# Kernel optimization log

Hardware: AMD Instinct MI355X
Metric: run time of the kernel (lower is better)

## Reference

```python
import jax, jax.numpy as jnp
import numpy as np

N_NODES = 50000
N_EDGES = 800000
K_HOPS = 3


def _gcn_norm(edge_index, num_nodes):
    # PyG gcn_norm with add_self_loops=False: sym normalization by target-degree
    row, col = edge_index[0], edge_index[1]  # source j -> target i
    ones = jnp.ones((edge_index.shape[1],), dtype=jnp.float32)
    deg = jax.ops.segment_sum(ones, col, num_segments=num_nodes)
    dinv = jnp.where(deg > 0, 1.0 / jnp.sqrt(deg), 0.0)
    return dinv[row] * dinv[col]  # [E]


def _propagate(h, row, col, norm, num_nodes):
    # out_i = sum_{j->i} norm_e * h_j   (scatter-add over edges)
    msg = h[row] * norm[:, None]  # [E, d]
    return jax.ops.segment_sum(msg, col, num_segments=num_nodes)


def _tag_conv(x, W, b, row, col, norm, num_nodes):
    # out = sum_{k=0..K} (A_norm^k x) @ W[k] + b
    out = x @ W[0]
    h = x
    for k in range(1, K_HOPS + 1):
        h = _propagate(h, row, col, norm, num_nodes)
        out = out + h @ W[k]
    return out + b


def setup_inputs() -> dict:
    key = jax.random.key(0)
    ks = jax.random.split(key, 12)
    x = jax.random.normal(ks[0], (N_NODES, 16), dtype=jnp.float32)
    edge_index = jax.random.randint(ks[1], (2, N_EDGES), 0, N_NODES, dtype=jnp.int64)
    dims = [(16, 64), (64, 64), (64, 64), (64, 64), (64, 4)]
    inp = {"x": x, "edge_index": edge_index}
    for i, (din, dout) in enumerate(dims):
        scale = 1.0 / np.sqrt(din)
        inp[f"W{i}"] = jax.random.normal(ks[2 + 2 * i], (K_HOPS + 1, din, dout), dtype=jnp.float32) * scale
        inp[f"b{i}"] = jnp.zeros((dout,), dtype=jnp.float32)
    return inp


def reference(x, edge_index, W0, b0, W1, b1, W2, b2, W3, b3, W4, b4):
    num_nodes = x.shape[0]
    row, col = edge_index[0], edge_index[1]
    norm = _gcn_norm(edge_index, num_nodes)
    Ws = [W0, W1, W2, W3, W4]
    bs = [b0, b1, b2, b3, b4]
    h = x
    for i in range(4):  # first len(convs)-1 layers: conv -> dropout(identity, eval) -> relu
        h = _tag_conv(h, Ws[i], bs[i], row, col, norm, num_nodes)
        h = jax.nn.relu(h)
    return _tag_conv(h, Ws[4], bs[4], row, col, norm, num_nodes)
```

## Files before the change

kernel.cpp:

```cpp
#include <hip/hip_runtime.h>
#include <hip/hip_fp16.h>

typedef _Float16 f16x8 __attribute__((ext_vector_type(8)));
typedef float f32x4 __attribute__((ext_vector_type(4)));

union H2I { int i; __half2 h; };
static __device__ inline float2 i2f2(int v) {
    H2I u; u.i = v; return __half22float2(u.h);
}
static __device__ inline int f2i2(float a, float b) {
    H2I u; u.h = __floats2half2_rn(a, b); return u.i;
}

struct F8 { float2 a, b, c, d; };
static __device__ inline void fma8(F8& s, int4 g, float w) {
    float2 t;
    t = i2f2(g.x); s.a.x += w * t.x; s.a.y += w * t.y;
    t = i2f2(g.y); s.b.x += w * t.x; s.b.y += w * t.y;
    t = i2f2(g.z); s.c.x += w * t.x; s.c.y += w * t.y;
    t = i2f2(g.w); s.d.x += w * t.x; s.d.y += w * t.y;
}


__global__ __launch_bounds__(256) void count_rank_kernel(const int* __restrict__ col,
                                                         int* __restrict__ cnt,
                                                         unsigned short* __restrict__ rank,
                                                         int E) {
    int e = blockIdx.x * 256 + threadIdx.x;
    if (e < E) rank[e] = (unsigned short)atomicAdd(&cnt[col[e]], 1);
}

__global__ __launch_bounds__(256) void scan_block_kernel(const int* __restrict__ cnt,
                                                         int* __restrict__ off,
                                                         int* __restrict__ bsum, int n) {
    const int gid = blockIdx.x * 256 + threadIdx.x;
    const int v = (gid < n) ? cnt[gid] : 0;
    const int lane = threadIdx.x & 63, w = threadIdx.x >> 6;
    int x = v;
#pragma unroll
    for (int d = 1; d < 64; d <<= 1) {
        int t = __shfl_up(x, d);
        if (lane >= d) x += t;
    }
    __shared__ int wt[4];
    if (lane == 63) wt[w] = x;
    __syncthreads();
    int base = 0;
#pragma unroll
    for (int i = 0; i < 3; ++i)
        if (i < w) base += wt[i];
    const int incl = base + x;
    if (gid < n) off[gid] = incl - v;
    if (threadIdx.x == 255) bsum[blockIdx.x] = incl;
}

__global__ __launch_bounds__(256) void scan_bsum_kernel(const int* __restrict__ bsum,
                                                        int* __restrict__ bbase, int nb) {
    const int tid = threadIdx.x;
    const int v = (tid < nb) ? bsum[tid] : 0;
    const int lane = tid & 63, w = tid >> 6;
    int x = v;
#pragma unroll
    for (int d = 1; d < 64; d <<= 1) {
        int t = __shfl_up(x, d);
        if (lane >= d) x += t;
    }
    __shared__ int wt[4];
    if (lane == 63) wt[w] = x;
    __syncthreads();
    int base = 0;
#pragma unroll
    for (int i = 0; i < 3; ++i)
        if (i < w) base += wt[i];
    if (tid < nb) bbase[tid] = base + x - v;
}

__global__ __launch_bounds__(256) void scan_apply_kernel(int* __restrict__ off,
                                                         const int* __restrict__ bbase,
                                                         int n, int E) {
    const int gid = blockIdx.x * 256 + threadIdx.x;
    if (gid < n) off[gid] += bbase[blockIdx.x];
    if (gid == n) off[n] = E;
}

__global__ __launch_bounds__(256) void prep_kernel(const int* __restrict__ cnt,
                                                   float* __restrict__ dinv,
                                                   const float* __restrict__ x,
                                                   __half* __restrict__ xcat,
                                                   const float* __restrict__ W0,
                                                   const float* __restrict__ W1,
                                                   const float* __restrict__ W2,
                                                   const float* __restrict__ W3,
                                                   __half* __restrict__ Bp0,
                                                   __half* __restrict__ Bp1,
                                                   __half* __restrict__ Bp2,
                                                   __half* __restrict__ Bp3, int N) {
    int t = blockIdx.x * 256 + threadIdx.x;
    if (t < N) {
        const int c = cnt[t];
        dinv[t] = (c > 0) ? 1.0f / sqrtf((float)c) : 0.0f;
        return;
    }
    t -= N;
    if (t < 2 * N) {
        const int n = t >> 1, q = t & 1;
        const float4 v0 = ((const float4*)x)[n * 4 + q * 2 + 0];
        const float4 v1 = ((const float4*)x)[n * 4 + q * 2 + 1];
        int4 o;
        o.x = f2i2(v0.x, v0.y);
        o.y = f2i2(v0.z, v0.w);
        o.z = f2i2(v1.x, v1.y);
        o.w = f2i2(v1.z, v1.w);
        ((int4*)xcat)[n * 8 + q] = o;
        return;
    }
    t -= 2 * N;
    const float* W;
    __half* Bp;
    if (t < 512) {
        W = W0; Bp = Bp0;
    } else if (t < 512 + 2048) {
        W = W1; Bp = Bp1; t -= 512;
    } else if (t < 512 + 2 * 2048) {
        W = W2; Bp = Bp2; t -= 512 + 2048;
    } else if (t < 512 + 3 * 2048) {
        W = W3; Bp = Bp3; t -= 512 + 2 * 2048;
    } else {
        return;
    }
    const int kk = t >> 8;
    const int nt = (t >> 6) & 3;
    const int l = t & 63;
    const int m = l & 15, kg = l >> 4;
    const int col = nt * 16 + m;
    __half tmp[8];
#pragma unroll
    for (int j = 0; j < 8; ++j) {
        const int k = kk * 32 + kg * 8 + j;
        tmp[j] = __float2half(W[k * 64 + col]);
    }
    ((int4*)Bp)[t] = *(int4*)tmp;
}

__global__ __launch_bounds__(256) void scatter_kernel(const int* __restrict__ row,
                                                      const int* __restrict__ col,
                                                      const int* __restrict__ off,
                                                      const unsigned short* __restrict__ rank,
                                                      const float* __restrict__ dinv,
                                                      int2* __restrict__ recs, int E) {
    int e = blockIdx.x * 256 + threadIdx.x;
    if (e >= E) return;
    const int r = row[e], c = col[e];
    const int pos = off[c] + (int)rank[e];
    recs[pos] = make_int2(r, __float_as_int(dinv[r] * dinv[c]));
}


template <int DQ, int S4>
__global__ __launch_bounds__(256) void gatherh_kernel(const int* __restrict__ off,
                                                      const int2* __restrict__ recs,
                                                      const __half* __restrict__ hin,
                                                      __half* __restrict__ hout, int nNodes) {
    const int t = blockIdx.x * 256 + threadIdx.x;
    const int n = t / DQ;
    const int q = t & (DQ - 1);
    if (n >= nNodes) return;
    const int4* __restrict__ h4 = (const int4*)hin;
    F8 s = {};
    int e = off[n];
    const int e1 = off[n + 1];
    for (; e + 8 <= e1; e += 8) {
        const int2 r0 = recs[e + 0];
        const int2 r1 = recs[e + 1];
        const int2 r2 = recs[e + 2];
        const int2 r3 = recs[e + 3];
        const int2 r4 = recs[e + 4];
        const int2 r5 = recs[e + 5];
        const int2 r6 = recs[e + 6];
        const int2 r7 = recs[e + 7];
        const int4 g0 = h4[r0.x * S4 + q];
        const int4 g1 = h4[r1.x * S4 + q];
        const int4 g2 = h4[r2.x * S4 + q];
        const int4 g3 = h4[r3.x * S4 + q];
        const int4 g4 = h4[r4.x * S4 + q];
        const int4 g5 = h4[r5.x * S4 + q];
        const int4 g6 = h4[r6.x * S4 + q];
        const int4 g7 = h4[r7.x * S4 + q];
        fma8(s, g0, __int_as_float(r0.y));
        fma8(s, g1, __int_as_float(r1.y));
        fma8(s, g2, __int_as_float(r2.y));
        fma8(s, g3, __int_as_float(r3.y));
        fma8(s, g4, __int_as_float(r4.y));
        fma8(s, g5, __int_as_float(r5.y));
        fma8(s, g6, __int_as_float(r6.y));
        fma8(s, g7, __int_as_float(r7.y));
    }
    for (; e + 4 <= e1; e += 4) {
        const int2 r0 = recs[e + 0];
        const int2 r1 = recs[e + 1];
        const int2 r2 = recs[e + 2];
        const int2 r3 = recs[e + 3];
        const int4 g0 = h4[r0.x * S4 + q];
        const int4 g1 = h4[r1.x * S4 + q];
        const int4 g2 = h4[r2.x * S4 + q];
        const int4 g3 = h4[r3.x * S4 + q];
        fma8(s, g0, __int_as_float(r0.y));
        fma8(s, g1, __int_as_float(r1.y));
        fma8(s, g2, __int_as_float(r2.y));
        fma8(s, g3, __int_as_float(r3.y));
    }
    for (; e < e1; ++e) {
        const int2 r = recs[e];
        fma8(s, h4[r.x * S4 + q], __int_as_float(r.y));
    }
    int4 o;
    o.x = f2i2(s.a.x, s.a.y);
    o.y = f2i2(s.b.x, s.b.y);
    o.z = f2i2(s.c.x, s.c.y);
    o.w = f2i2(s.d.x, s.d.y);
    ((int4*)hout)[n * S4 + q] = o;
}


template <int K>
__global__ __launch_bounds__(256) void gemmcat_mfma(const __half* __restrict__ A,
                                                    const __half* __restrict__ Bp,
                                                    const float* __restrict__ bias,
                                                    __half* __restrict__ out, int N) {
    __shared__ __half hs[128][72];
    const int wave = threadIdx.x >> 6;
    const int lane = threadIdx.x & 63;
    const int nb = blockIdx.x * 128 + wave * 32;
    const int m = lane & 15;
    const int kg = lane >> 4;

    const int row0 = min(nb + m, N - 1);
    const int row1 = min(nb + 16 + m, N - 1);
    const f16x8* a0p = (const f16x8*)(A + (size_t)row0 * K + kg * 8);
    const f16x8* a1p = (const f16x8*)(A + (size_t)row1 * K + kg * 8);
    const f16x8* bp = (const f16x8*)Bp + lane;

    f32x4 acc[2][4];
#pragma unroll
    for (int nt = 0; nt < 4; ++nt) {
        const float bv = bias[nt * 16 + m];
        acc[0][nt] = (f32x4){bv, bv, bv, bv};
        acc[1][nt] = (f32x4){bv, bv, bv, bv};
    }

#pragma unroll
    for (int kk = 0; kk < K / 32; ++kk) {
        const f16x8 a0 = a0p[kk * 4];
        const f16x8 a1 = a1p[kk * 4];
#pragma unroll
        for (int nt = 0; nt < 4; ++nt) {
            const f16x8 b = bp[(kk * 4 + nt) * 64];
            acc[0][nt] = __builtin_amdgcn_mfma_f32_16x16x32_f16(a0, b, acc[0][nt], 0, 0, 0);
            acc[1][nt] = __builtin_amdgcn_mfma_f32_16x16x32_f16(a1, b, acc[1][nt], 0, 0, 0);
        }
    }

#pragma unroll
    for (int mt = 0; mt < 2; ++mt) {
#pragma unroll
        for (int nt = 0; nt < 4; ++nt) {
#pragma unroll
            for (int r = 0; r < 4; ++r) {
                const int nl = wave * 32 + mt * 16 + kg * 4 + r;
                hs[nl][nt * 16 + m] = __float2half(fmaxf(acc[mt][nt][r], 0.f));
            }
        }
    }
    __syncthreads();
    const int nl = threadIdx.x >> 1;
    const int seg = threadIdx.x & 1;
    const int node = blockIdx.x * 128 + nl;
    if (node >= N) return;
    const int4* src = (const int4*)&hs[nl][seg * 32];
    int4* dst = (int4*)(out + (size_t)node * 256 + seg * 32);
    dst[0] = src[0];
    dst[1] = src[1];
    dst[2] = src[2];
    dst[3] = src[3];
}


__global__ __launch_bounds__(256) void proj4h_kernel(const __half* __restrict__ h,
                                                     const float* __restrict__ W,
                                                     float* __restrict__ P0,
                                                     float* __restrict__ P1,
                                                     float* __restrict__ P2,
                                                     float* __restrict__ P3, int nNodes) {
    __shared__ float Ws[4 * 64 * 4];
    for (int i = threadIdx.x; i < 1024; i += 256) Ws[i] = W[i];
    __syncthreads();
    const int k = threadIdx.x & 3;
    const int n = blockIdx.x * 64 + (threadIdx.x >> 2);
    if (n >= nNodes) return;
    const int4* __restrict__ h8 = (const int4*)h + (size_t)n * 32;
    const float4* W4 = (const float4*)(Ws + k * 256);
    float4 acc = make_float4(0.f, 0.f, 0.f, 0.f);
#pragma unroll
    for (int i8 = 0; i8 < 8; ++i8) {
        const int4 g = h8[i8];
        const float2 f0 = i2f2(g.x), f1 = i2f2(g.y), f2v = i2f2(g.z), f3 = i2f2(g.w);
        const float hv[8] = {f0.x, f0.y, f1.x, f1.y, f2v.x, f2v.y, f3.x, f3.y};
#pragma unroll
        for (int j = 0; j < 8; ++j) {
            const float4 wr = W4[i8 * 8 + j];
            acc.x += hv[j] * wr.x;
            acc.y += hv[j] * wr.y;
            acc.z += hv[j] * wr.z;
            acc.w += hv[j] * wr.w;
        }
    }
    float4* dst = (k == 0) ? (float4*)P0 : (k == 1) ? (float4*)P1 : (k == 2) ? (float4*)P2
                                                                             : (float4*)P3;
    dst[n] = acc;
}

template <bool FINAL>
__global__ __launch_bounds__(256) void prop1_add_kernel(const int* __restrict__ off,
                                                        const int2* __restrict__ recs,
                                                        const float* __restrict__ Uin,
                                                        const float* __restrict__ P,
                                                        const float* __restrict__ b,
                                                        float* __restrict__ out, int nNodes) {
    const int n = blockIdx.x * 256 + threadIdx.x;
    if (n >= nNodes) return;
    const float4* __restrict__ u4 = (const float4*)Uin;
    float4 acc = ((const float4*)P)[n];
    if (FINAL) {
        const float4 bv = *(const float4*)b;
        acc.x += bv.x;
        acc.y += bv.y;
        acc.z += bv.z;
        acc.w += bv.w;
    }
    int e = off[n];
    const int e1 = off[n + 1];
    for (; e + 4 <= e1; e += 4) {
        const int2 r0 = recs[e + 0];
        const int2 r1 = recs[e + 1];
        const int2 r2 = recs[e + 2];
        const int2 r3 = recs[e + 3];
        const float4 a = u4[r0.x], bb = u4[r1.x], c = u4[r2.x], d = u4[r3.x];
        const float w0 = __int_as_float(r0.y), w1 = __int_as_float(r1.y);
        const float w2 = __int_as_float(r2.y), w3 = __int_as_float(r3.y);
        acc.x += w0 * a.x + w1 * bb.x + w2 * c.x + w3 * d.x;
        acc.y += w0 * a.y + w1 * bb.y + w2 * c.y + w3 * d.y;
        acc.z += w0 * a.z + w1 * bb.z + w2 * c.z + w3 * d.z;
        acc.w += w0 * a.w + w1 * bb.w + w2 * c.w + w3 * d.w;
    }
    for (; e < e1; ++e) {
        const int2 r = recs[e];
        const float ww = __int_as_float(r.y);
        const float4 hv = u4[r.x];
        acc.x += ww * hv.x;
        acc.y += ww * hv.y;
        acc.z += ww * hv.z;
        acc.w += ww * hv.w;
    }
    ((float4*)out)[n] = acc;
}


extern "C" void kernel_launch(void* const* d_in, const int* in_sizes, int n_in,
                              void* d_out, int out_size, void* d_ws, size_t ws_size,
                              hipStream_t stream) {
    const float* x = (const float*)d_in[0];
    const int* ei = (const int*)d_in[1];
    const float* W[5] = {(const float*)d_in[2], (const float*)d_in[4], (const float*)d_in[6],
                         (const float*)d_in[8], (const float*)d_in[10]};
    const float* bb[5] = {(const float*)d_in[3], (const float*)d_in[5], (const float*)d_in[7],
                          (const float*)d_in[9], (const float*)d_in[11]};
    const int E = in_sizes[1] / 2;
    const int N = in_sizes[0] / 16;
    float* outp = (float*)d_out;

    char* p = (char*)d_ws;
    auto alloc = [&](size_t bytes) {
        char* r = p;
        p += (bytes + 255) & ~size_t(255);
        return r;
    };
    const int nb = (N + 255) / 256;
    int* cnt = (int*)alloc((size_t)N * 4);
    int* off = (int*)alloc((size_t)(N + 1) * 4);
    float* dinv = (float*)alloc((size_t)N * 4);
    int* bsum = (int*)alloc((size_t)nb * 4);
    int* bbase = (int*)alloc((size_t)nb * 4);
    unsigned short* rank = (unsigned short*)alloc((size_t)E * 2);
    int2* recs = (int2*)alloc((size_t)E * 8);
    __half* xcat = (__half*)alloc((size_t)N * 64 * 2);
    __half* hcatA = (__half*)alloc((size_t)N * 256 * 2);
    __half* hcatB = (__half*)alloc((size_t)N * 256 * 2);
    __half* Bp0 = (__half*)alloc((size_t)512 * 8 * 2);
    __half* Bp1 = (__half*)alloc((size_t)2048 * 8 * 2);
    __half* Bp2 = (__half*)alloc((size_t)2048 * 8 * 2);
    __half* Bp3 = (__half*)alloc((size_t)2048 * 8 * 2);
    float* P0 = (float*)alloc((size_t)N * 4 * 4);
    float* P1 = (float*)alloc((size_t)N * 4 * 4);
    float* P2 = (float*)alloc((size_t)N * 4 * 4);
    float* P3 = (float*)alloc((size_t)N * 4 * 4);
    float* Ua = (float*)alloc((size_t)N * 4 * 4);
    float* Ub = (float*)alloc((size_t)N * 4 * 4);

    hipMemsetAsync(cnt, 0, (size_t)N * 4, stream);
    const int eb = (E + 255) / 256;
    count_rank_kernel<<<eb, 256, 0, stream>>>(ei + E, cnt, rank, E);
    scan_block_kernel<<<nb, 256, 0, stream>>>(cnt, off, bsum, N);
    scan_bsum_kernel<<<1, 256, 0, stream>>>(bsum, bbase, nb);
    scan_apply_kernel<<<nb, 256, 0, stream>>>(off, bbase, N, E);
    const int prep_total = 3 * N + 512 + 3 * 2048;
    prep_kernel<<<(prep_total + 255) / 256, 256, 0, stream>>>(
        cnt, dinv, x, xcat, W[0], W[1], W[2], W[3], Bp0, Bp1, Bp2, Bp3, N);
    scatter_kernel<<<eb, 256, 0, stream>>>(ei, ei + E, off, rank, dinv, recs, E);

    const int gh2 = (N * 2 + 255) / 256;
    const int gh8 = (N * 8 + 255) / 256;
    const int gm = (N + 127) / 128;
    const int gq = (N + 63) / 64;
    const int p1 = (N + 255) / 256;

    gatherh_kernel<2, 8><<<gh2, 256, 0, stream>>>(off, recs, xcat + 0, xcat + 16, N);
    gatherh_kernel<2, 8><<<gh2, 256, 0, stream>>>(off, recs, xcat + 16, xcat + 32, N);
    gatherh_kernel<2, 8><<<gh2, 256, 0, stream>>>(off, recs, xcat + 32, xcat + 48, N);
    gemmcat_mfma<64><<<gm, 256, 0, stream>>>(xcat, Bp0, bb[0], hcatA, N);

    __half* cur = hcatA;
    __half* nxt = hcatB;
    const __half* Bps[4] = {nullptr, Bp1, Bp2, Bp3};
    for (int l = 1; l <= 3; ++l) {
        gatherh_kernel<8, 32><<<gh8, 256, 0, stream>>>(off, recs, cur + 0, cur + 64, N);
        gatherh_kernel<8, 32><<<gh8, 256, 0, stream>>>(off, recs, cur + 64, cur + 128, N);
        gatherh_kernel<8, 32><<<gh8, 256, 0, stream>>>(off, recs, cur + 128, cur + 192, N);
        gemmcat_mfma<256><<<gm, 256, 0, stream>>>(cur, Bps[l], bb[l], nxt, N);
        __half* t = cur;
        cur = nxt;
        nxt = t;
    }

    proj4h_kernel<<<gq, 256, 0, stream>>>(cur, W[4], P0, P1, P2, P3, N);
    prop1_add_kernel<false><<<p1, 256, 0, stream>>>(off, recs, P3, P2, nullptr, Ua, N);
    prop1_add_kernel<false><<<p1, 256, 0, stream>>>(off, recs, Ua, P1, nullptr, Ub, N);
    prop1_add_kernel<true><<<p1, 256, 0, stream>>>(off, recs, Ub, P0, bb[4], outp, N);
}
```

Baseline: 336.5 us.

## Split each node's edges across lanes and pack edge records into 32 bits

The gather and propagation kernels now give each node a lane group that walks its edge list in parallel and combines partial sums with cross-lane shuffle reductions. Before, one thread walked a node's edges in sequence. Edge records are compressed from 8 bytes to 4: a 17-bit source index plus a truncated fp16 weight, which halves record traffic. The separate block-sum scan kernel is dropped, so each block now adds up its own preceding block sums. The aim is better load balance and memory-level parallelism on the skewed edge lists, at the cost of lanes idling on short lists, less precise weights, and a node-index limit of 2^17.

```diff
diff --git a/kernel.cpp b/kernel.cpp
--- a/kernel.cpp
+++ b/kernel.cpp
@@ -11,14 +11,10 @@
 static __device__ inline int f2i2(float a, float b) {
     H2I u; u.h = __floats2half2_rn(a, b); return u.i;
 }
-
-struct F8 { float2 a, b, c, d; };
-static __device__ inline void fma8(F8& s, int4 g, float w) {
-    float2 t;
-    t = i2f2(g.x); s.a.x += w * t.x; s.a.y += w * t.y;
-    t = i2f2(g.y); s.b.x += w * t.x; s.b.y += w * t.y;
-    t = i2f2(g.z); s.c.x += w * t.x; s.c.y += w * t.y;
-    t = i2f2(g.w); s.d.x += w * t.x; s.d.y += w * t.y;
+static __device__ inline float hbits2f(unsigned int b) {
+    union { unsigned short s; __half h; } u;
+    u.s = (unsigned short)b;
+    return __half2float(u.h);
 }
 
 
@@ -54,32 +50,21 @@
     if (threadIdx.x == 255) bsum[blockIdx.x] = incl;
 }
 
-__global__ __launch_bounds__(256) void scan_bsum_kernel(const int* __restrict__ bsum,
-                                                        int* __restrict__ bbase, int nb) {
+__global__ __launch_bounds__(256) void scan_apply_kernel(int* __restrict__ off,
+                                                         const int* __restrict__ bsum,
+                                                         int n, int E) {
+    __shared__ int sbase;
     const int tid = threadIdx.x;
-    const int v = (tid < nb) ? bsum[tid] : 0;
-    const int lane = tid & 63, w = tid >> 6;
-    int x = v;
-#pragma unroll
-    for (int d = 1; d < 64; d <<= 1) {
-        int t = __shfl_up(x, d);
-        if (lane >= d) x += t;
-    }
-    __shared__ int wt[4];
-    if (lane == 63) wt[w] = x;
+    if (tid < 64) {
+        int s = 0;
+        for (int i = tid; i < blockIdx.x; i += 64) s += bsum[i];
+#pragma unroll
+        for (int d = 1; d < 64; d <<= 1) s += __shfl_xor(s, d);
+        if (tid == 0) sbase = s;
+    }
     __syncthreads();
-    int base = 0;
-#pragma unroll
-    for (int i = 0; i < 3; ++i)
-        if (i < w) base += wt[i];
-    if (tid < nb) bbase[tid] = base + x - v;
-}
-
-__global__ __launch_bounds__(256) void scan_apply_kernel(int* __restrict__ off,
-                                                         const int* __restrict__ bbase,
-                                                         int n, int E) {
-    const int gid = blockIdx.x * 256 + threadIdx.x;
-    if (gid < n) off[gid] += bbase[blockIdx.x];
+    const int gid = blockIdx.x * 256 + tid;
+    if (gid < n) off[gid] += sbase;
     if (gid == n) off[n] = E;
 }
 
@@ -147,78 +132,57 @@
                                                       const int* __restrict__ off,
                                                       const unsigned short* __restrict__ rank,
                                                       const float* __restrict__ dinv,
-                                                      int2* __restrict__ recs, int E) {
+                                                      unsigned int* __restrict__ recs, int E) {
     int e = blockIdx.x * 256 + threadIdx.x;
     if (e >= E) return;
     const int r = row[e], c = col[e];
     const int pos = off[c] + (int)rank[e];
-    recs[pos] = make_int2(r, __float_as_int(dinv[r] * dinv[c]));
-}
-
-
-template <int DQ, int S4>
-__global__ __launch_bounds__(256) void gatherh_kernel(const int* __restrict__ off,
-                                                      const int2* __restrict__ recs,
+    const unsigned int nb = (unsigned int)__half_as_ushort(__float2half_rn(dinv[r] * dinv[c]));
+    recs[pos] = ((unsigned int)r << 15) | (nb >> 1);
+}
+
+
+template <int ES, int Q, int S4>
+__global__ __launch_bounds__(256) void gatherw_kernel(const int* __restrict__ off,
+                                                      const unsigned int* __restrict__ recs,
                                                       const __half* __restrict__ hin,
                                                       __half* __restrict__ hout, int nNodes) {
-    const int t = blockIdx.x * 256 + threadIdx.x;
-    const int n = t / DQ;
-    const int q = t & (DQ - 1);
+    constexpr int GS = ES * Q;
+    constexpr int NPW = 64 / GS;
+    const int wid = (blockIdx.x * 256 + threadIdx.x) >> 6;
+    const int lane = threadIdx.x & 63;
+    const int n = wid * NPW + lane / GS;
     if (n >= nNodes) return;
+    const int gl = lane % GS;
+    const int es = gl / Q;
+    const int q = gl % Q;
     const int4* __restrict__ h4 = (const int4*)hin;
-    F8 s = {};
-    int e = off[n];
-    const int e1 = off[n + 1];
-    for (; e + 8 <= e1; e += 8) {
-        const int2 r0 = recs[e + 0];
-        const int2 r1 = recs[e + 1];
-        const int2 r2 = recs[e + 2];
-        const int2 r3 = recs[e + 3];
-        const int2 r4 = recs[e + 4];
-        const int2 r5 = recs[e + 5];
-        const int2 r6 = recs[e + 6];
-        const int2 r7 = recs[e + 7];
-        const int4 g0 = h4[r0.x * S4 + q];
-        const int4 g1 = h4[r1.x * S4 + q];
-        const int4 g2 = h4[r2.x * S4 + q];
-        const int4 g3 = h4[r3.x * S4 + q];
-        const int4 g4 = h4[r4.x * S4 + q];
-        const int4 g5 = h4[r5.x * S4 + q];
-        const int4 g6 = h4[r6.x * S4 + q];
-        const int4 g7 = h4[r7.x * S4 + q];
-        fma8(s, g0, __int_as_float(r0.y));
-        fma8(s, g1, __int_as_float(r1.y));
-        fma8(s, g2, __int_as_float(r2.y));
-        fma8(s, g3, __int_as_float(r3.y));
-        fma8(s, g4, __int_as_float(r4.y));
-        fma8(s, g5, __int_as_float(r5.y));
-        fma8(s, g6, __int_as_float(r6.y));
-        fma8(s, g7, __int_as_float(r7.y));
-    }
-    for (; e + 4 <= e1; e += 4) {
-        const int2 r0 = recs[e + 0];
-        const int2 r1 = recs[e + 1];
-        const int2 r2 = recs[e + 2];
-        const int2 r3 = recs[e + 3];
-        const int4 g0 = h4[r0.x * S4 + q];
-        const int4 g1 = h4[r1.x * S4 + q];
-        const int4 g2 = h4[r2.x * S4 + q];
-        const int4 g3 = h4[r3.x * S4 + q];
-        fma8(s, g0, __int_as_float(r0.y));
-        fma8(s, g1, __int_as_float(r1.y));
-        fma8(s, g2, __int_as_float(r2.y));
-        fma8(s, g3, __int_as_float(r3.y));
-    }
-    for (; e < e1; ++e) {
-        const int2 r = recs[e];
-        fma8(s, h4[r.x * S4 + q], __int_as_float(r.y));
-    }
-    int4 o;
-    o.x = f2i2(s.a.x, s.a.y);
-    o.y = f2i2(s.b.x, s.b.y);
-    o.z = f2i2(s.c.x, s.c.y);
-    o.w = f2i2(s.d.x, s.d.y);
-    ((int4*)hout)[n * S4 + q] = o;
+    const int e0 = off[n], e1 = off[n + 1];
+    float acc[8] = {0.f, 0.f, 0.f, 0.f, 0.f, 0.f, 0.f, 0.f};
+    for (int base = e0; base < e1; base += ES) {
+        const int ee = base + es;
+        const unsigned int r = (ee < e1) ? recs[ee] : 0u;
+        const float w = hbits2f((r & 0x7FFFu) << 1);
+        const int4 g = h4[(size_t)(r >> 15) * S4 + q];
+        float2 t;
+        t = i2f2(g.x); acc[0] += w * t.x; acc[1] += w * t.y;
+        t = i2f2(g.y); acc[2] += w * t.x; acc[3] += w * t.y;
+        t = i2f2(g.z); acc[4] += w * t.x; acc[5] += w * t.y;
+        t = i2f2(g.w); acc[6] += w * t.x; acc[7] += w * t.y;
+    }
+#pragma unroll
+    for (int d = Q; d < GS; d <<= 1) {
+#pragma unroll
+        for (int j = 0; j < 8; ++j) acc[j] += __shfl_xor(acc[j], d);
+    }
+    if (gl < Q) {
+        int4 o;
+        o.x = f2i2(acc[0], acc[1]);
+        o.y = f2i2(acc[2], acc[3]);
+        o.z = f2i2(acc[4], acc[5]);
+        o.w = f2i2(acc[6], acc[7]);
+        ((int4*)hout)[(size_t)n * S4 + q] = o;
+    }
 }
 
 
@@ -320,48 +284,52 @@
 }
 
 template <bool FINAL>
-__global__ __launch_bounds__(256) void prop1_add_kernel(const int* __restrict__ off,
-                                                        const int2* __restrict__ recs,
-                                                        const float* __restrict__ Uin,
-                                                        const float* __restrict__ P,
-                                                        const float* __restrict__ b,
-                                                        float* __restrict__ out, int nNodes) {
-    const int n = blockIdx.x * 256 + threadIdx.x;
+__global__ __launch_bounds__(256) void prop1w_kernel(const int* __restrict__ off,
+                                                     const unsigned int* __restrict__ recs,
+                                                     const float* __restrict__ Uin,
+                                                     const float* __restrict__ P,
+                                                     const float* __restrict__ b,
+                                                     float* __restrict__ out, int nNodes) {
+    const int wid = (blockIdx.x * 256 + threadIdx.x) >> 6;
+    const int lane = threadIdx.x & 63;
+    const int n = wid * 4 + (lane >> 4);
     if (n >= nNodes) return;
+    const int es = lane & 15;
     const float4* __restrict__ u4 = (const float4*)Uin;
-    float4 acc = ((const float4*)P)[n];
-    if (FINAL) {
-        const float4 bv = *(const float4*)b;
-        acc.x += bv.x;
-        acc.y += bv.y;
-        acc.z += bv.z;
-        acc.w += bv.w;
-    }
-    int e = off[n];
-    const int e1 = off[n + 1];
-    for (; e + 4 <= e1; e += 4) {
-        const int2 r0 = recs[e + 0];
-        const int2 r1 = recs[e + 1];
-        const int2 r2 = recs[e + 2];
-        const int2 r3 = recs[e + 3];
-        const float4 a = u4[r0.x], bb = u4[r1.x], c = u4[r2.x], d = u4[r3.x];
-        const float w0 = __int_as_float(r0.y), w1 = __int_as_float(r1.y);
-        const float w2 = __int_as_float(r2.y), w3 = __int_as_float(r3.y);
-        acc.x += w0 * a.x + w1 * bb.x + w2 * c.x + w3 * d.x;
-        acc.y += w0 * a.y + w1 * bb.y + w2 * c.y + w3 * d.y;
-        acc.z += w0 * a.z + w1 * bb.z + w2 * c.z + w3 * d.z;
-        acc.w += w0 * a.w + w1 * bb.w + w2 * c.w + w3 * d.w;
-    }
-    for (; e < e1; ++e) {
-        const int2 r = recs[e];
-        const float ww = __int_as_float(r.y);
-        const float4 hv = u4[r.x];
-        acc.x += ww * hv.x;
-        acc.y += ww * hv.y;
-        acc.z += ww * hv.z;
-        acc.w += ww * hv.w;
-    }
-    ((float4*)out)[n] = acc;
+    const int e0 = off[n], e1 = off[n + 1];
+    float4 acc = make_float4(0.f, 0.f, 0.f, 0.f);
+    for (int base = e0; base < e1; base += 16) {
+        const int ee = base + es;
+        const unsigned int r = (ee < e1) ? recs[ee] : 0u;
+        const float w = hbits2f((r & 0x7FFFu) << 1);
+        const float4 u = u4[r >> 15];
+        acc.x += w * u.x;
+        acc.y += w * u.y;
+        acc.z += w * u.z;
+        acc.w += w * u.w;
+    }
+#pragma unroll
+    for (int d = 1; d < 16; d <<= 1) {
+        acc.x += __shfl_xor(acc.x, d);
+        acc.y += __shfl_xor(acc.y, d);
+        acc.z += __shfl_xor(acc.z, d);
+        acc.w += __shfl_xor(acc.w, d);
+    }
+    if (es == 0) {
+        const float4 pv = ((const float4*)P)[n];
+        acc.x += pv.x;
+        acc.y += pv.y;
+        acc.z += pv.z;
+        acc.w += pv.w;
+        if (FINAL) {
+            const float4 bv = *(const float4*)b;
+            acc.x += bv.x;
+            acc.y += bv.y;
+            acc.z += bv.z;
+            acc.w += bv.w;
+        }
+        ((float4*)out)[n] = acc;
+    }
 }
 
 
@@ -389,9 +357,8 @@
     int* off = (int*)alloc((size_t)(N + 1) * 4);
     float* dinv = (float*)alloc((size_t)N * 4);
     int* bsum = (int*)alloc((size_t)nb * 4);
-    int* bbase = (int*)alloc((size_t)nb * 4);
     unsigned short* rank = (unsigned short*)alloc((size_t)E * 2);
-    int2* recs = (int2*)alloc((size_t)E * 8);
+    unsigned int* recs = (unsigned int*)alloc((size_t)E * 4);
     __half* xcat = (__half*)alloc((size_t)N * 64 * 2);
     __half* hcatA = (__half*)alloc((size_t)N * 256 * 2);
     __half* hcatB = (__half*)alloc((size_t)N * 256 * 2);
@@ -410,31 +377,30 @@
     const int eb = (E + 255) / 256;
     count_rank_kernel<<<eb, 256, 0, stream>>>(ei + E, cnt, rank, E);
     scan_block_kernel<<<nb, 256, 0, stream>>>(cnt, off, bsum, N);
-    scan_bsum_kernel<<<1, 256, 0, stream>>>(bsum, bbase, nb);
-    scan_apply_kernel<<<nb, 256, 0, stream>>>(off, bbase, N, E);
+    scan_apply_kernel<<<nb, 256, 0, stream>>>(off, bsum, N, E);
     const int prep_total = 3 * N + 512 + 3 * 2048;
     prep_kernel<<<(prep_total + 255) / 256, 256, 0, stream>>>(
         cnt, dinv, x, xcat, W[0], W[1], W[2], W[3], Bp0, Bp1, Bp2, Bp3, N);
     scatter_kernel<<<eb, 256, 0, stream>>>(ei, ei + E, off, rank, dinv, recs, E);
 
-    const int gh2 = (N * 2 + 255) / 256;
-    const int gh8 = (N * 8 + 255) / 256;
+    const int gw64 = (N * 64 + 255) / 256;
+    const int gw16 = (((N + 1) / 2) * 64 + 255) / 256;
+    const int gw4 = (((N + 3) / 4) * 64 + 255) / 256;
     const int gm = (N + 127) / 128;
     const int gq = (N + 63) / 64;
-    const int p1 = (N + 255) / 256;
-
-    gatherh_kernel<2, 8><<<gh2, 256, 0, stream>>>(off, recs, xcat + 0, xcat + 16, N);
-    gatherh_kernel<2, 8><<<gh2, 256, 0, stream>>>(off, recs, xcat + 16, xcat + 32, N);
-    gatherh_kernel<2, 8><<<gh2, 256, 0, stream>>>(off, recs, xcat + 32, xcat + 48, N);
+
+    gatherw_kernel<16, 2, 8><<<gw16, 256, 0, stream>>>(off, recs, xcat + 0, xcat + 16, N);
+    gatherw_kernel<16, 2, 8><<<gw16, 256, 0, stream>>>(off, recs, xcat + 16, xcat + 32, N);
+    gatherw_kernel<16, 2, 8><<<gw16, 256, 0, stream>>>(off, recs, xcat + 32, xcat + 48, N);
     gemmcat_mfma<64><<<gm, 256, 0, stream>>>(xcat, Bp0, bb[0], hcatA, N);
 
     __half* cur = hcatA;
     __half* nxt = hcatB;
     const __half* Bps[4] = {nullptr, Bp1, Bp2, Bp3};
     for (int l = 1; l <= 3; ++l) {
-        gatherh_kernel<8, 32><<<gh8, 256, 0, stream>>>(off, recs, cur + 0, cur + 64, N);
-        gatherh_kernel<8, 32><<<gh8, 256, 0, stream>>>(off, recs, cur + 64, cur + 128, N);
-        gatherh_kernel<8, 32><<<gh8, 256, 0, stream>>>(off, recs, cur + 128, cur + 192, N);
+        gatherw_kernel<8, 8, 32><<<gw64, 256, 0, stream>>>(off, recs, cur + 0, cur + 64, N);
+        gatherw_kernel<8, 8, 32><<<gw64, 256, 0, stream>>>(off, recs, cur + 64, cur + 128, N);
+        gatherw_kernel<8, 8, 32><<<gw64, 256, 0, stream>>>(off, recs, cur + 128, cur + 192, N);
         gemmcat_mfma<256><<<gm, 256, 0, stream>>>(cur, Bps[l], bb[l], nxt, N);
         __half* t = cur;
         cur = nxt;
@@ -442,7 +408,7 @@
     }
 
     proj4h_kernel<<<gq, 256, 0, stream>>>(cur, W[4], P0, P1, P2, P3, N);
-    prop1_add_kernel<false><<<p1, 256, 0, stream>>>(off, recs, P3, P2, nullptr, Ua, N);
-    prop1_add_kernel<false><<<p1, 256, 0, stream>>>(off, recs, Ua, P1, nullptr, Ub, N);
-    prop1_add_kernel<true><<<p1, 256, 0, stream>>>(off, recs, Ub, P0, bb[4], outp, N);
-}
+    prop1w_kernel<false><<<gw4, 256, 0, stream>>>(off, recs, P3, P2, nullptr, Ua, N);
+    prop1w_kernel<false><<<gw4, 256, 0, stream>>>(off, recs, Ua, P1, nullptr, Ub, N);
+    prop1w_kernel<true><<<gw4, 256, 0, stream>>>(off, recs, Ub, P0, bb[4], outp, N);
+}
```

Result: slower. 381.5 us (+13.4%).
